# Kernel tuning notes

Hardware: AMD Instinct MI355X
Metric: run time of the kernel (lower is better)

The kernel has to match this reference:

```python
import jax, jax.numpy as jnp
import numpy as np

N = 50000      # nodes
E = 1600000    # edges (avg degree 32)
C_IN = 128
C_H = 128
C_OUT = 10
G = 512        # number of graphs in the batch


def setup_inputs() -> dict:
    key = jax.random.key(0)
    ks = jax.random.split(key, 16)
    x = jax.random.normal(ks[0], (N, C_IN), dtype=jnp.float32)
    edge_index = jax.random.randint(ks[1], (2, E), 0, N, dtype=jnp.int64)
    batch = jnp.sort(jax.random.randint(ks[2], (N,), 0, G, dtype=jnp.int64))

    def lin(k, fan_in, fan_out):
        lim = 1.0 / np.sqrt(fan_in)
        return jax.random.uniform(k, (fan_in, fan_out), jnp.float32, -lim, lim)

    return {
        "x": x, "edge_index": edge_index, "batch": batch,
        # conv1: c_in -> c_hidden
        "Wr1": lin(ks[3], C_IN, C_H), "br1": jnp.zeros((C_H,), jnp.float32),
        "Wo1": lin(ks[4], C_IN, C_H),
        # conv2: c_hidden -> 2*c_hidden
        "Wr2": lin(ks[5], C_H, 2 * C_H), "br2": jnp.zeros((2 * C_H,), jnp.float32),
        "Wo2": lin(ks[6], C_H, 2 * C_H),
        # conv3: 2*c_hidden -> c_hidden
        "Wr3": lin(ks[7], 2 * C_H, C_H), "br3": jnp.zeros((C_H,), jnp.float32),
        "Wo3": lin(ks[8], 2 * C_H, C_H),
        # head
        "W1": lin(ks[9], C_H, 4 * C_OUT), "b1": jnp.zeros((4 * C_OUT,), jnp.float32),
        "W2": lin(ks[10], 4 * C_OUT, C_OUT), "b2": jnp.zeros((C_OUT,), jnp.float32),
    }


def _graph_conv(x, src, dst, Wr, br, Wo):
    # PyG GraphConv: lin_rel(sum_{j in N(i)} x_j) + lin_root(x_i)
    agg = jax.ops.segment_sum(x[src], dst, num_segments=N)  # [N, F_in]
    return agg @ Wr + br + x @ Wo


def reference(x, edge_index, batch, Wr1, br1, Wo1, Wr2, br2, Wo2,
              Wr3, br3, Wo3, W1, b1, W2, b2):
    src, dst = edge_index[0], edge_index[1]
    h = jax.nn.relu(_graph_conv(x, src, dst, Wr1, br1, Wo1))
    h = jax.nn.relu(_graph_conv(h, src, dst, Wr2, br2, Wo2))
    h = _graph_conv(h, src, dst, Wr3, br3, Wo3)
    # global mean pool over graphs
    sums = jax.ops.segment_sum(h, batch, num_segments=G)            # [G, C_H]
    cnts = jax.ops.segment_sum(jnp.ones((N,), h.dtype), batch, num_segments=G)
    pooled = sums / jnp.maximum(cnts, 1.0)[:, None]
    # dropout is identity in eval mode
    out = pooled @ W1 + b1
    out = out @ W2 + b2
    return out
```

## Files before the change

kernel.cpp:

```cpp
#include <hip/hip_runtime.h>
#include <hip/hip_bf16.h>
#include <cstddef>

#define NN 50000
#define EE 1600000
#define GG 512
#define NB 196
#define BSTRIDE 16384
#define BCAP 10240
#define XBLKS 6250
#define SCBLKS 782
#define PSEG 8

typedef unsigned int u32;
typedef unsigned short u16;
typedef __attribute__((ext_vector_type(8))) short frag_ab;
typedef __attribute__((ext_vector_type(4))) float frag_cd;
typedef __attribute__((ext_vector_type(2))) float f32x2;

__device__ __forceinline__ void gl_lds16(const void* g, void* l) {
    __builtin_amdgcn_global_load_lds(
        (const __attribute__((address_space(1))) u32*)g,
        (__attribute__((address_space(3))) u32*)l, 16, 0, 0);
}
__device__ __forceinline__ float b2f_lo(u32 v) { return __uint_as_float(v << 16); }
__device__ __forceinline__ float b2f_hi(u32 v) { return __uint_as_float(v & 0xffff0000u); }
__device__ __forceinline__ float b2f(u32 v, int odd) { return odd ? b2f_hi(v) : b2f_lo(v); }
__device__ __forceinline__ u16 f2b(float x) {
    __hip_bfloat16 h = __float2bfloat16(x);
    return *(u16*)&h;
}
__device__ __forceinline__ u32 pack2(float lo, float hi) {
    return ((u32)f2b(hi) << 16) | f2b(lo);
}
__device__ __forceinline__ void accf8(float* a, u32 w) {
    f32x2 p0 = __builtin_amdgcn_cvt_pk_f32_fp8(w, false);
    f32x2 p1 = __builtin_amdgcn_cvt_pk_f32_fp8(w, true);
    a[0] += p0.x; a[1] += p0.y; a[2] += p1.x; a[3] += p1.y;
}
__device__ __forceinline__ u32 pk4_f8(float a, float b, float c, float d) {
    u32 w = __builtin_amdgcn_cvt_pk_fp8_f32(a, b, 0, false);
    return __builtin_amdgcn_cvt_pk_fp8_f32(c, d, w, true);
}

__device__ inline int lower_bound_i(const int* a, int n, int v) {
    int lo = 0, hi = n;
    while (lo < hi) {
        int m = (lo + hi) >> 1;
        if (a[m] < v) lo = m + 1; else hi = m;
    }
    return lo;
}



__global__ __launch_bounds__(256) void bscatter_prep_kernel(
    const int* __restrict__ ei, int* __restrict__ bcnt, u32* __restrict__ pairs,
    const float* __restrict__ x, u16* __restrict__ ax, u32* __restrict__ x8,
    const float* __restrict__ Wr1, const float* __restrict__ Wo1,
    const float* __restrict__ Wr2, const float* __restrict__ Wo2,
    const float* __restrict__ Wr3, const float* __restrict__ Wo3,
    const float* __restrict__ br3,
    u16* __restrict__ BT1, u16* __restrict__ BT2, u16* __restrict__ BT3,
    float* __restrict__ bias3, const int* __restrict__ batch,
    int* __restrict__ gn) {
    __shared__ int lcnt[NB];
    __shared__ int lbase[NB];
    __shared__ unsigned short lpos[2048];
    int bid = blockIdx.x, t = threadIdx.x;
    if (bid < SCBLKS) {
        int e0 = bid * 2048;
        u32 pk[8];
        int bk[8];
        for (int i = t; i < NB; i += 256) lcnt[i] = 0;
        __syncthreads();
#pragma unroll
        for (int i = 0; i < 8; ++i) {
            int e = e0 + i * 256 + t;
            if (e < EE) {
                int dst = ei[EE + e], src = ei[e];
                int b = dst >> 8;
                bk[i] = b;
                pk[i] = ((u32)src << 8) | (u32)(dst & 255);
                lpos[i * 256 + t] = (unsigned short)atomicAdd(&lcnt[b], 1);
            } else bk[i] = -1;
        }
        __syncthreads();
        for (int i = t; i < NB; i += 256) lbase[i] = atomicAdd(&bcnt[i], lcnt[i]);
        __syncthreads();
#pragma unroll
        for (int i = 0; i < 8; ++i) {
            if (bk[i] >= 0) {
                int pos = lbase[bk[i]] + (int)lpos[i * 256 + t];
                pairs[(size_t)bk[i] * BSTRIDE + pos] = pk[i];
            }
        }
    } else if (bid < SCBLKS + XBLKS) {
        int idx = (bid - SCBLKS) * 256 + t;
        int row = idx >> 5, q = idx & 31;
        float4 v = *(const float4*)(x + (size_t)row * 128 + q * 4);
        *(u32*)(ax + (size_t)row * 256 + 128 + q * 4) = pack2(v.x, v.y);
        *(u32*)(ax + (size_t)row * 256 + 128 + q * 4 + 2) = pack2(v.z, v.w);
        x8[(size_t)row * 32 + q] = pk4_f8(v.x, v.y, v.z, v.w);
    } else if (bid < SCBLKS + XBLKS + 256) {
        int m = bid - SCBLKS - XBLKS;
        int k = t;
        BT2[m * 256 + k] = f2b(k < 128 ? Wr2[k * 256 + m] : Wo2[(k - 128) * 256 + m]);
        BT3[m * 256 + k] = f2b(m < 128 ? Wr3[k * 128 + m] : Wo3[k * 128 + (m - 128)]);
        if (m < 128)
            BT1[m * 256 + k] = f2b(k < 128 ? Wr1[k * 128 + m] : Wo1[(k - 128) * 128 + m]);
        if (k == 0) bias3[m] = (m < 128) ? 0.f : br3[m - 128];
    } else {
        int g = (bid - SCBLKS - XBLKS - 256) * 256 + t;
        if (g <= GG) gn[g] = lower_bound_i(batch, NN, g);
    }
}


__global__ __launch_bounds__(1024) void bfill_kernel(const u32* __restrict__ pairs,
                                                     const int* __restrict__ bcnt,
                                                     int* __restrict__ ofs,
                                                     u16* __restrict__ srcl) {
    __shared__ int sc[256];
    __shared__ int cnts[256];
    __shared__ int lcnt[256];
    __shared__ int lcur[256];
    __shared__ int lbuf[BCAP];
    int b = blockIdx.x, t = threadIdx.x;
    if (t < 256) {
        int c = (t < NB) ? bcnt[t] : 0;
        cnts[t] = c;
        sc[t] = c;
        lcnt[t] = 0;
    }
    __syncthreads();
    for (int off = 1; off < 256; off <<= 1) {
        int v = (t >= off && t < 256) ? sc[t - off] : 0;
        __syncthreads();
        if (t < 256) sc[t] += v;
        __syncthreads();
    }
    int base = sc[b] - cnts[b];
    int span = cnts[b];
    const u32* pp = pairs + (size_t)b * BSTRIDE;
    for (int j = t; j < span; j += 1024) atomicAdd(&lcnt[pp[j] & 255u], 1);
    __syncthreads();
    int nc = 0;
    if (t < 256) {
        nc = lcnt[t];
        sc[t] = nc;
    }
    __syncthreads();
    for (int off = 1; off < 256; off <<= 1) {
        int v = (t >= off && t < 256) ? sc[t - off] : 0;
        __syncthreads();
        if (t < 256) sc[t] += v;
        __syncthreads();
    }
    if (t < 256) {
        int excl = sc[t] - nc;
        int node = b * 256 + t;
        if (node < NN) ofs[node] = base + excl;
        lcur[t] = excl;
    }
    if (b == 0 && t == 256) ofs[NN] = EE;
    __syncthreads();
    for (int j = t; j < span; j += 1024) {
        u32 p = pp[j];
        int pos = atomicAdd(&lcur[p & 255u], 1);
        int src = (int)(p >> 8);
        if (pos < BCAP) lbuf[pos] = src;
        else srcl[base + pos] = (u16)src;
    }
    __syncthreads();
    int lim = span < BCAP ? span : BCAP;
    for (int j = t; j < lim; j += 1024) srcl[base + j] = (u16)lbuf[j];
}


__global__ __launch_bounds__(256) void pull_f8_kernel(const u32* __restrict__ X8,
                                                      const int* __restrict__ ofs,
                                                      const u16* __restrict__ srcl,
                                                      u32* __restrict__ outu) {
    int node = (blockIdx.x * 256 + threadIdx.x) >> 6;
    int lane = threadIdx.x & 63;
    int q = lane >> 3, l = lane & 7;
    int lo = ofs[node], hi = ofs[node + 1];
    float acc[16];
#pragma unroll
    for (int i = 0; i < 16; ++i) acc[i] = 0.f;
    int j = lo;
    for (; j + 31 < hi; j += 32) {
        int s0 = srcl[j + q], s1 = srcl[j + 8 + q];
        int s2 = srcl[j + 16 + q], s3 = srcl[j + 24 + q];
        uint4 v0 = *(const uint4*)(X8 + (size_t)s0 * 32 + l * 4);
        uint4 v1 = *(const uint4*)(X8 + (size_t)s1 * 32 + l * 4);
        uint4 v2 = *(const uint4*)(X8 + (size_t)s2 * 32 + l * 4);
        uint4 v3 = *(const uint4*)(X8 + (size_t)s3 * 32 + l * 4);
        accf8(acc + 0, v0.x); accf8(acc + 4, v0.y); accf8(acc + 8, v0.z); accf8(acc + 12, v0.w);
        accf8(acc + 0, v1.x); accf8(acc + 4, v1.y); accf8(acc + 8, v1.z); accf8(acc + 12, v1.w);
        accf8(acc + 0, v2.x); accf8(acc + 4, v2.y); accf8(acc + 8, v2.z); accf8(acc + 12, v2.w);
        accf8(acc + 0, v3.x); accf8(acc + 4, v3.y); accf8(acc + 8, v3.z); accf8(acc + 12, v3.w);
    }
    if (j + 15 < hi) {
        int s0 = srcl[j + q], s1 = srcl[j + 8 + q];
        uint4 v0 = *(const uint4*)(X8 + (size_t)s0 * 32 + l * 4);
        uint4 v1 = *(const uint4*)(X8 + (size_t)s1 * 32 + l * 4);
        accf8(acc + 0, v0.x); accf8(acc + 4, v0.y); accf8(acc + 8, v0.z); accf8(acc + 12, v0.w);
        accf8(acc + 0, v1.x); accf8(acc + 4, v1.y); accf8(acc + 8, v1.z); accf8(acc + 12, v1.w);
        j += 16;
    }
    if (j + 7 < hi) {
        int s = srcl[j + q];
        uint4 v = *(const uint4*)(X8 + (size_t)s * 32 + l * 4);
        accf8(acc + 0, v.x); accf8(acc + 4, v.y); accf8(acc + 8, v.z); accf8(acc + 12, v.w);
        j += 8;
    }
    if (j + q < hi) {
        int s = srcl[j + q];
        uint4 v = *(const uint4*)(X8 + (size_t)s * 32 + l * 4);
        accf8(acc + 0, v.x); accf8(acc + 4, v.y); accf8(acc + 8, v.z); accf8(acc + 12, v.w);
    }
#pragma unroll
    for (int i = 0; i < 16; ++i) {
        acc[i] += __shfl_xor(acc[i], 8, 64);
        acc[i] += __shfl_xor(acc[i], 16, 64);
        acc[i] += __shfl_xor(acc[i], 32, 64);
    }
    if (q == 0) {
        uint4 r0, r1;
        r0.x = pack2(acc[0], acc[1]);  r0.y = pack2(acc[2], acc[3]);
        r0.z = pack2(acc[4], acc[5]);  r0.w = pack2(acc[6], acc[7]);
        r1.x = pack2(acc[8], acc[9]);  r1.y = pack2(acc[10], acc[11]);
        r1.z = pack2(acc[12], acc[13]); r1.w = pack2(acc[14], acc[15]);
        *(uint4*)(outu + (size_t)node * 128 + l * 8) = r0;
        *(uint4*)(outu + (size_t)node * 128 + l * 8 + 4) = r1;
    }
}


__global__ __launch_bounds__(256, 3) void gemm1_kernel(
    const u16* __restrict__ A, const u16* __restrict__ BT1,
    const float* __restrict__ br1, u16* __restrict__ C, u32* __restrict__ F8) {
    __shared__ alignas(16) u16 As[64 * 32];
    __shared__ alignas(16) u16 Bs[128 * 32];
    __shared__ alignas(16) u16 Hs[64 * 128];
    const int t = threadIdx.x;
    const int lane = t & 63, w = t >> 6;
    const int quad = lane >> 4, l16 = lane & 15;
    const int row0 = blockIdx.x * 64;

    const int ra = t >> 2, oa = (t & 3) * 8;
    const int garow = min(row0 + ra, NN - 1);
    const size_t gA = (size_t)garow * 256 + oa;
    size_t gB[2];
#pragma unroll
    for (int i = 0; i < 2; ++i) {
        int cbi = i * 256 + t;
        gB[i] = (size_t)(cbi >> 2) * 256 + (cbi & 3) * 8;
    }

    frag_cd acc[8];
#pragma unroll
    for (int i = 0; i < 8; ++i) acc[i] = (frag_cd)0.f;

    for (int kk = 0; kk < 256; kk += 32) {
        __syncthreads();
        gl_lds16(A + gA + kk, &As[t * 8]);
#pragma unroll
        for (int i = 0; i < 2; ++i)
            gl_lds16(BT1 + gB[i] + kk, &Bs[(i * 256 + t) * 8]);
        __syncthreads();
        frag_ab a = *(const frag_ab*)&As[(w * 16 + l16) * 32 + quad * 8];
#pragma unroll
        for (int nt = 0; nt < 8; ++nt) {
            frag_ab b = *(const frag_ab*)&Bs[(nt * 16 + l16) * 32 + quad * 8];
            acc[nt] = __builtin_amdgcn_mfma_f32_16x16x32_bf16(a, b, acc[nt], 0, 0, 0);
        }
    }
#pragma unroll
    for (int nt = 0; nt < 8; ++nt) {
        int col = nt * 16 + l16;
        float bv = br1[col];
#pragma unroll
        for (int r = 0; r < 4; ++r) {
            int lr = w * 16 + quad * 4 + r;
            float v = fmaxf(acc[nt][r] + bv, 0.f);
            Hs[(lr * 128 + col) ^ ((lr & 7) << 3)] = f2b(v);
        }
    }
    __syncthreads();
    const uint4* Hs128 = (const uint4*)Hs;
#pragma unroll
    for (int it = 0; it < 4; ++it) {
        int row = it * 16 + (t >> 4);
        int grp = t & 15;
        uint4 v = Hs128[row * 16 + (grp ^ (row & 7))];
        int grow = row0 + row;
        if (grow < NN) {
            *(uint4*)(C + (size_t)grow * 256 + 128 + grp * 8) = v;
            float f0 = b2f_lo(v.x), f1 = b2f_hi(v.x), f2 = b2f_lo(v.y), f3 = b2f_hi(v.y);
            float f4 = b2f_lo(v.z), f5 = b2f_hi(v.z), f6 = b2f_lo(v.w), f7 = b2f_hi(v.w);
            uint2 w8;
            w8.x = pk4_f8(f0, f1, f2, f3);
            w8.y = pk4_f8(f4, f5, f6, f7);
            *(uint2*)(F8 + (size_t)grow * 32 + grp * 2) = w8;
        }
    }
}


__global__ __launch_bounds__(256, 3) void gemm23_kernel(
    const u16* __restrict__ A, const u16* __restrict__ BT2,
    const float* __restrict__ br2, const u16* __restrict__ BT3,
    const float* __restrict__ bias3, u16* __restrict__ C, u32* __restrict__ T8) {
    __shared__ alignas(16) u16 As[64 * 32];
    __shared__ alignas(16) u16 Bs[256 * 32];
    __shared__ alignas(16) u16 Hs[64 * 256];
    const int t = threadIdx.x;
    const int lane = t & 63, w = t >> 6;
    const int quad = lane >> 4, l16 = lane & 15;
    const int row0 = blockIdx.x * 64;

    const int ra = t >> 2, oa = (t & 3) * 8;
    const int garow = min(row0 + ra, NN - 1);
    const size_t gA = (size_t)garow * 256 + oa;
    size_t gB[4];
#pragma unroll
    for (int i = 0; i < 4; ++i) {
        int cbi = i * 256 + t;
        gB[i] = (size_t)(cbi >> 2) * 256 + (cbi & 3) * 8;
    }

    frag_cd acc[16];
#pragma unroll
    for (int i = 0; i < 16; ++i) acc[i] = (frag_cd)0.f;

    for (int kk = 0; kk < 256; kk += 32) {
        __syncthreads();
        gl_lds16(A + gA + kk, &As[t * 8]);
#pragma unroll
        for (int i = 0; i < 4; ++i)
            gl_lds16(BT2 + gB[i] + kk, &Bs[(i * 256 + t) * 8]);
        __syncthreads();
        frag_ab a = *(const frag_ab*)&As[(w * 16 + l16) * 32 + quad * 8];
#pragma unroll
        for (int nt = 0; nt < 16; ++nt) {
            frag_ab b = *(const frag_ab*)&Bs[(nt * 16 + l16) * 32 + quad * 8];
            acc[nt] = __builtin_amdgcn_mfma_f32_16x16x32_bf16(a, b, acc[nt], 0, 0, 0);
        }
    }
#pragma unroll
    for (int nt = 0; nt < 16; ++nt) {
        int col = nt * 16 + l16;
        float bv = br2[col];
#pragma unroll
        for (int r = 0; r < 4; ++r) {
            int lr = w * 16 + quad * 4 + r;
            float v = fmaxf(acc[nt][r] + bv, 0.f);
            Hs[(lr * 256 + col) ^ ((lr & 7) << 3)] = f2b(v);
        }
    }

#pragma unroll
    for (int i = 0; i < 16; ++i) acc[i] = (frag_cd)0.f;
    const int hrow = w * 16 + l16;
    for (int kk = 0; kk < 256; kk += 32) {
        __syncthreads();
#pragma unroll
        for (int i = 0; i < 4; ++i)
            gl_lds16(BT3 + gB[i] + kk, &Bs[(i * 256 + t) * 8]);
        __syncthreads();
        frag_ab a = *(const frag_ab*)&Hs[(hrow * 256 + kk + quad * 8) ^
                                         ((hrow & 7) << 3)];
#pragma unroll
        for (int nt = 0; nt < 16; ++nt) {
            frag_ab b = *(const frag_ab*)&Bs[(nt * 16 + l16) * 32 + quad * 8];
            acc[nt] = __builtin_amdgcn_mfma_f32_16x16x32_bf16(a, b, acc[nt], 0, 0, 0);
        }
    }

#pragma unroll
    for (int nt = 0; nt < 16; ++nt) {
        int col = nt * 16 + l16;
        float bv = bias3[col];
#pragma unroll
        for (int r = 0; r < 4; ++r) {
            int lr = w * 16 + quad * 4 + r;
            Hs[(lr * 256 + col) ^ ((lr & 7) << 3)] = f2b(acc[nt][r] + bv);
        }
    }
    __syncthreads();
    const uint4* Hs128 = (const uint4*)Hs;
#pragma unroll
    for (int it = 0; it < 8; ++it) {
        int row = it * 8 + (t >> 5);
        int grp = t & 31;
        uint4 v = Hs128[row * 32 + (grp ^ (row & 7))];
        int grow = row0 + row;
        if (grow < NN)
            *(uint4*)(C + (size_t)grow * 256 + grp * 8) = v;
    }
#pragma unroll
    for (int it = 0; it < 4; ++it) {
        int row = it * 16 + (t >> 4);
        int grp = t & 15;
        uint4 v = Hs128[row * 32 + (grp ^ (row & 7))];
        int grow = row0 + row;
        if (grow < NN) {
            float f0 = b2f_lo(v.x), f1 = b2f_hi(v.x), f2 = b2f_lo(v.y), f3 = b2f_hi(v.y);
            float f4 = b2f_lo(v.z), f5 = b2f_hi(v.z), f6 = b2f_lo(v.w), f7 = b2f_hi(v.w);
            uint2 w8;
            w8.x = pk4_f8(f0, f1, f2, f3);
            w8.y = pk4_f8(f4, f5, f6, f7);
            *(uint2*)(T8 + (size_t)grow * 32 + grp * 2) = w8;
        }
    }
}


__global__ __launch_bounds__(256) void pool3_f8_kernel(
    const u32* __restrict__ T8, const u32* __restrict__ Tu,
    const int* __restrict__ ofs, const u16* __restrict__ srcl,
    const int* __restrict__ gn, float* __restrict__ psum) {
    __shared__ float red[4][128];
    __shared__ float po[2][128];
    int gb = blockIdx.x;
    int g = gb >> 3, s = gb & 7;
    int t = threadIdx.x;
    int w = t >> 6, lane = t & 63;
    int q = lane >> 3, l = lane & 7;
    int n_lo = gn[g], n_hi = gn[g + 1];
    int glo = ofs[n_lo], ghi = ofs[n_hi];
    int len = ghi - glo;
    int s_lo = glo + (int)(((long long)len * s) >> 3);
    int s_hi = glo + (int)(((long long)len * (s + 1)) >> 3);
    int slen = s_hi - s_lo;
    int wlo = s_lo + ((slen * w) >> 2);
    int whi = s_lo + ((slen * (w + 1)) >> 2);

    float acc[16];
#pragma unroll
    for (int i = 0; i < 16; ++i) acc[i] = 0.f;
    int j = wlo;
    for (; j + 31 < whi; j += 32) {
        int s0 = srcl[j + q], s1 = srcl[j + 8 + q];
        int s2 = srcl[j + 16 + q], s3 = srcl[j + 24 + q];
        uint4 v0 = *(const uint4*)(T8 + (size_t)s0 * 32 + l * 4);
        uint4 v1 = *(const uint4*)(T8 + (size_t)s1 * 32 + l * 4);
        uint4 v2 = *(const uint4*)(T8 + (size_t)s2 * 32 + l * 4);
        uint4 v3 = *(const uint4*)(T8 + (size_t)s3 * 32 + l * 4);
        accf8(acc + 0, v0.x); accf8(acc + 4, v0.y); accf8(acc + 8, v0.z); accf8(acc + 12, v0.w);
        accf8(acc + 0, v1.x); accf8(acc + 4, v1.y); accf8(acc + 8, v1.z); accf8(acc + 12, v1.w);
        accf8(acc + 0, v2.x); accf8(acc + 4, v2.y); accf8(acc + 8, v2.z); accf8(acc + 12, v2.w);
        accf8(acc + 0, v3.x); accf8(acc + 4, v3.y); accf8(acc + 8, v3.z); accf8(acc + 12, v3.w);
    }
    if (j + 15 < whi) {
        int s0 = srcl[j + q], s1 = srcl[j + 8 + q];
        uint4 v0 = *(const uint4*)(T8 + (size_t)s0 * 32 + l * 4);
        uint4 v1 = *(const uint4*)(T8 + (size_t)s1 * 32 + l * 4);
        accf8(acc + 0, v0.x); accf8(acc + 4, v0.y); accf8(acc + 8, v0.z); accf8(acc + 12, v0.w);
        accf8(acc + 0, v1.x); accf8(acc + 4, v1.y); accf8(acc + 8, v1.z); accf8(acc + 12, v1.w);
        j += 16;
    }
    if (j + 7 < whi) {
        int sv = srcl[j + q];
        uint4 v = *(const uint4*)(T8 + (size_t)sv * 32 + l * 4);
        accf8(acc + 0, v.x); accf8(acc + 4, v.y); accf8(acc + 8, v.z); accf8(acc + 12, v.w);
        j += 8;
    }
    if (j + q < whi) {
        int sv = srcl[j + q];
        uint4 v = *(const uint4*)(T8 + (size_t)sv * 32 + l * 4);
        accf8(acc + 0, v.x); accf8(acc + 4, v.y); accf8(acc + 8, v.z); accf8(acc + 12, v.w);
    }
#pragma unroll
    for (int i = 0; i < 16; ++i) {
        acc[i] += __shfl_xor(acc[i], 8, 64);
        acc[i] += __shfl_xor(acc[i], 16, 64);
        acc[i] += __shfl_xor(acc[i], 32, 64);
    }
    if (q == 0) {
#pragma unroll
        for (int i = 0; i < 16; ++i) red[w][l * 16 + i] = acc[i];
    }
    float so = 0.f;
    int ch = t & 127, rg = t >> 7;
    for (int r = n_lo + s * 2 + rg; r < n_hi; r += 16)
        so += b2f(Tu[(size_t)r * 128 + 64 + (ch >> 1)], ch & 1);
    po[rg][ch] = so;
    __syncthreads();
    if (t < 128) {
        float v = red[0][t] + red[1][t] + red[2][t] + red[3][t] + po[0][t] + po[1][t];
        psum[((size_t)g * PSEG + s) * 128 + t] = v;
    }
}


__global__ __launch_bounds__(128) void head_kernel(
    const float* __restrict__ psum, const int* __restrict__ gn,
    const float* __restrict__ W1, const float* __restrict__ b1,
    const float* __restrict__ W2, const float* __restrict__ b2,
    float* __restrict__ out) {
    __shared__ float p[128];
    __shared__ float hid[40];
    int g = blockIdx.x, t = threadIdx.x;
    int cnt = gn[g + 1] - gn[g];
    float sv = 0.f;
#pragma unroll
    for (int k = 0; k < PSEG; ++k) sv += psum[((size_t)g * PSEG + k) * 128 + t];
    p[t] = sv / fmaxf((float)cnt, 1.f);
    __syncthreads();
    if (t < 40) {
        float v = b1[t];
        for (int k = 0; k < 128; ++k) v += p[k] * W1[k * 40 + t];
        hid[t] = v;
    }
    __syncthreads();
    if (t < 10) {
        float v = b2[t];
        for (int j = 0; j < 40; ++j) v += hid[j] * W2[j * 10 + t];
        out[g * 10 + t] = v;
    }
}


extern "C" void kernel_launch(void* const* d_in, const int* in_sizes, int n_in,
                              void* d_out, int out_size, void* d_ws, size_t ws_size,
                              hipStream_t stream) {
    const float* x   = (const float*)d_in[0];
    const int* ei    = (const int*)d_in[1];
    const int* batch = (const int*)d_in[2];
    const float* Wr1 = (const float*)d_in[3];
    const float* br1 = (const float*)d_in[4];
    const float* Wo1 = (const float*)d_in[5];
    const float* Wr2 = (const float*)d_in[6];
    const float* br2 = (const float*)d_in[7];
    const float* Wo2 = (const float*)d_in[8];
    const float* Wr3 = (const float*)d_in[9];
    const float* br3 = (const float*)d_in[10];
    const float* Wo3 = (const float*)d_in[11];
    const float* W1  = (const float*)d_in[12];
    const float* b1  = (const float*)d_in[13];
    const float* W2  = (const float*)d_in[14];
    const float* b2  = (const float*)d_in[15];
    float* out = (float*)d_out;

    char* ws = (char*)d_ws;
    size_t off = 0;
    auto alloc = [&](size_t bytes) {
        void* p = ws + off;
        off += (bytes + 255) & ~(size_t)255;
        return p;
    };
    int* ofs      = (int*)alloc((NN + 1) * sizeof(int));
    int* bcnt     = (int*)alloc(256 * sizeof(int));
    int* gn       = (int*)alloc((GG + 1) * sizeof(int));
    u16* srcl     = (u16*)alloc((size_t)EE * 2);
    u16* ax       = (u16*)alloc((size_t)NN * 256 * 2);
    u16* ah1      = (u16*)alloc((size_t)NN * 256 * 2);
    u16* t3o3     = (u16*)alloc((size_t)NN * 256 * 2);
    u32* x8       = (u32*)alloc((size_t)NN * 128);
    u32* h1f8     = (u32*)alloc((size_t)NN * 128);
    u32* t3f8     = (u32*)alloc((size_t)NN * 128);
    float* psum   = (float*)alloc((size_t)GG * PSEG * 128 * sizeof(float));
    u16* BT1      = (u16*)alloc(128 * 256 * 2);
    u16* BT2      = (u16*)alloc(256 * 256 * 2);
    u16* BT3      = (u16*)alloc(256 * 256 * 2);
    float* bias3  = (float*)alloc(256 * sizeof(float));
    u32* pairs = (u32*)t3o3;

    hipMemsetAsync(bcnt, 0, 256 * sizeof(int), stream);

    bscatter_prep_kernel<<<SCBLKS + XBLKS + 256 + 3, 256, 0, stream>>>(
        ei, bcnt, pairs, x, ax, x8, Wr1, Wo1, Wr2, Wo2, Wr3, Wo3, br3,
        BT1, BT2, BT3, bias3, batch, gn);
    bfill_kernel<<<NB, 1024, 0, stream>>>(pairs, bcnt, ofs, srcl);

    pull_f8_kernel<<<NN * 64 / 256, 256, 0, stream>>>(x8, ofs, srcl, (u32*)ax);
    gemm1_kernel<<<782, 256, 0, stream>>>(ax, BT1, br1, ah1, h1f8);
    pull_f8_kernel<<<NN * 64 / 256, 256, 0, stream>>>(h1f8, ofs, srcl, (u32*)ah1);
    gemm23_kernel<<<782, 256, 0, stream>>>(ah1, BT2, br2, BT3, bias3, t3o3, t3f8);

    pool3_f8_kernel<<<GG * PSEG, 256, 0, stream>>>(t3f8, (const u32*)t3o3,
                                                   ofs, srcl, gn, psum);
    head_kernel<<<GG, 128, 0, stream>>>(psum, gn, W1, b1, W2, b2, out);
}
```

Before: 301.3 us.

## Double-buffer LDS tiles in GEMM kernels to overlap loads with MFMA

Both GEMM kernels now keep two LDS buffers for the A/B tiles. The next k-slice is prefetched while MFMAs run on the current one, cutting one barrier per iteration, and the layer-3 weight prefetch is chained onto the end of the layer-2 loop. Occupancy hints change (gemm1 up to 4 blocks per CU, gemm23 down to 2) because LDS use grows. The fp8 epilogue is merged into the bf16 store loop so Hs is read once. The larger LDS footprint may lower occupancy for gemm23, and these GEMMs are probably a small part of a runtime dominated by the gather/scatter kernels.

After: 296.6 us. No clear change (-1.6%).

```diff
diff --git a/kernel.cpp b/kernel.cpp
--- a/kernel.cpp
+++ b/kernel.cpp
@@ -239,11 +239,11 @@
 }
 
 
-__global__ __launch_bounds__(256, 3) void gemm1_kernel(
+__global__ __launch_bounds__(256, 4) void gemm1_kernel(
     const u16* __restrict__ A, const u16* __restrict__ BT1,
     const float* __restrict__ br1, u16* __restrict__ C, u32* __restrict__ F8) {
-    __shared__ alignas(16) u16 As[64 * 32];
-    __shared__ alignas(16) u16 Bs[128 * 32];
+    __shared__ alignas(16) u16 As[2][64 * 32];
+    __shared__ alignas(16) u16 Bs[2][128 * 32];
     __shared__ alignas(16) u16 Hs[64 * 128];
     const int t = threadIdx.x;
     const int lane = t & 63, w = t >> 6;
@@ -264,19 +264,28 @@
 #pragma unroll
     for (int i = 0; i < 8; ++i) acc[i] = (frag_cd)0.f;
 
+    gl_lds16(A + gA, &As[0][t * 8]);
+#pragma unroll
+    for (int i = 0; i < 2; ++i)
+        gl_lds16(BT1 + gB[i], &Bs[0][(i * 256 + t) * 8]);
+    __syncthreads();
+
+    int buf = 0;
     for (int kk = 0; kk < 256; kk += 32) {
-        __syncthreads();
-        gl_lds16(A + gA + kk, &As[t * 8]);
-#pragma unroll
-        for (int i = 0; i < 2; ++i)
-            gl_lds16(BT1 + gB[i] + kk, &Bs[(i * 256 + t) * 8]);
-        __syncthreads();
-        frag_ab a = *(const frag_ab*)&As[(w * 16 + l16) * 32 + quad * 8];
+        if (kk < 224) {
+            gl_lds16(A + gA + kk + 32, &As[buf ^ 1][t * 8]);
+#pragma unroll
+            for (int i = 0; i < 2; ++i)
+                gl_lds16(BT1 + gB[i] + kk + 32, &Bs[buf ^ 1][(i * 256 + t) * 8]);
+        }
+        frag_ab a = *(const frag_ab*)&As[buf][(w * 16 + l16) * 32 + quad * 8];
 #pragma unroll
         for (int nt = 0; nt < 8; ++nt) {
-            frag_ab b = *(const frag_ab*)&Bs[(nt * 16 + l16) * 32 + quad * 8];
+            frag_ab b = *(const frag_ab*)&Bs[buf][(nt * 16 + l16) * 32 + quad * 8];
             acc[nt] = __builtin_amdgcn_mfma_f32_16x16x32_bf16(a, b, acc[nt], 0, 0, 0);
         }
+        __syncthreads();
+        buf ^= 1;
     }
 #pragma unroll
     for (int nt = 0; nt < 8; ++nt) {
@@ -310,12 +319,12 @@
 }
 
 
-__global__ __launch_bounds__(256, 3) void gemm23_kernel(
+__global__ __launch_bounds__(256, 2) void gemm23_kernel(
     const u16* __restrict__ A, const u16* __restrict__ BT2,
     const float* __restrict__ br2, const u16* __restrict__ BT3,
     const float* __restrict__ bias3, u16* __restrict__ C, u32* __restrict__ T8) {
-    __shared__ alignas(16) u16 As[64 * 32];
-    __shared__ alignas(16) u16 Bs[256 * 32];
+    __shared__ alignas(16) u16 As[2][64 * 32];
+    __shared__ alignas(16) u16 Bs[2][256 * 32];
     __shared__ alignas(16) u16 Hs[64 * 256];
     const int t = threadIdx.x;
     const int lane = t & 63, w = t >> 6;
@@ -336,19 +345,32 @@
 #pragma unroll
     for (int i = 0; i < 16; ++i) acc[i] = (frag_cd)0.f;
 
+    gl_lds16(A + gA, &As[0][t * 8]);
+#pragma unroll
+    for (int i = 0; i < 4; ++i)
+        gl_lds16(BT2 + gB[i], &Bs[0][(i * 256 + t) * 8]);
+    __syncthreads();
+
+    int buf = 0;
     for (int kk = 0; kk < 256; kk += 32) {
-        __syncthreads();
-        gl_lds16(A + gA + kk, &As[t * 8]);
-#pragma unroll
-        for (int i = 0; i < 4; ++i)
-            gl_lds16(BT2 + gB[i] + kk, &Bs[(i * 256 + t) * 8]);
-        __syncthreads();
-        frag_ab a = *(const frag_ab*)&As[(w * 16 + l16) * 32 + quad * 8];
+        if (kk < 224) {
+            gl_lds16(A + gA + kk + 32, &As[buf ^ 1][t * 8]);
+#pragma unroll
+            for (int i = 0; i < 4; ++i)
+                gl_lds16(BT2 + gB[i] + kk + 32, &Bs[buf ^ 1][(i * 256 + t) * 8]);
+        } else {
+#pragma unroll
+            for (int i = 0; i < 4; ++i)
+                gl_lds16(BT3 + gB[i], &Bs[buf ^ 1][(i * 256 + t) * 8]);
+        }
+        frag_ab a = *(const frag_ab*)&As[buf][(w * 16 + l16) * 32 + quad * 8];
 #pragma unroll
         for (int nt = 0; nt < 16; ++nt) {
-            frag_ab b = *(const frag_ab*)&Bs[(nt * 16 + l16) * 32 + quad * 8];
+            frag_ab b = *(const frag_ab*)&Bs[buf][(nt * 16 + l16) * 32 + quad * 8];
             acc[nt] = __builtin_amdgcn_mfma_f32_16x16x32_bf16(a, b, acc[nt], 0, 0, 0);
         }
+        __syncthreads();
+        buf ^= 1;
     }
 #pragma unroll
     for (int nt = 0; nt < 16; ++nt) {
@@ -366,18 +388,20 @@
     for (int i = 0; i < 16; ++i) acc[i] = (frag_cd)0.f;
     const int hrow = w * 16 + l16;
     for (int kk = 0; kk < 256; kk += 32) {
-        __syncthreads();
-#pragma unroll
-        for (int i = 0; i < 4; ++i)
-            gl_lds16(BT3 + gB[i] + kk, &Bs[(i * 256 + t) * 8]);
-        __syncthreads();
+        if (kk < 224) {
+#pragma unroll
+            for (int i = 0; i < 4; ++i)
+                gl_lds16(BT3 + gB[i] + kk + 32, &Bs[buf ^ 1][(i * 256 + t) * 8]);
+        }
         frag_ab a = *(const frag_ab*)&Hs[(hrow * 256 + kk + quad * 8) ^
                                          ((hrow & 7) << 3)];
 #pragma unroll
         for (int nt = 0; nt < 16; ++nt) {
-            frag_ab b = *(const frag_ab*)&Bs[(nt * 16 + l16) * 32 + quad * 8];
+            frag_ab b = *(const frag_ab*)&Bs[buf][(nt * 16 + l16) * 32 + quad * 8];
             acc[nt] = __builtin_amdgcn_mfma_f32_16x16x32_bf16(a, b, acc[nt], 0, 0, 0);
         }
+        __syncthreads();
+        buf ^= 1;
     }
 
 #pragma unroll
@@ -398,22 +422,16 @@
         int grp = t & 31;
         uint4 v = Hs128[row * 32 + (grp ^ (row & 7))];
         int grow = row0 + row;
-        if (grow < NN)
+        if (grow < NN) {
             *(uint4*)(C + (size_t)grow * 256 + grp * 8) = v;
-    }
-#pragma unroll
-    for (int it = 0; it < 4; ++it) {
-        int row = it * 16 + (t >> 4);
-        int grp = t & 15;
-        uint4 v = Hs128[row * 32 + (grp ^ (row & 7))];
-        int grow = row0 + row;
-        if (grow < NN) {
-            float f0 = b2f_lo(v.x), f1 = b2f_hi(v.x), f2 = b2f_lo(v.y), f3 = b2f_hi(v.y);
-            float f4 = b2f_lo(v.z), f5 = b2f_hi(v.z), f6 = b2f_lo(v.w), f7 = b2f_hi(v.w);
-            uint2 w8;
-            w8.x = pk4_f8(f0, f1, f2, f3);
-            w8.y = pk4_f8(f4, f5, f6, f7);
-            *(uint2*)(T8 + (size_t)grow * 32 + grp * 2) = w8;
+            if (grp < 16) {
+                float f0 = b2f_lo(v.x), f1 = b2f_hi(v.x), f2 = b2f_lo(v.y), f3 = b2f_hi(v.y);
+                float f4 = b2f_lo(v.z), f5 = b2f_hi(v.z), f6 = b2f_lo(v.w), f7 = b2f_hi(v.w);
+                uint2 w8;
+                w8.x = pk4_f8(f0, f1, f2, f3);
+                w8.y = pk4_f8(f4, f5, f6, f7);
+                *(uint2*)(T8 + (size_t)grow * 32 + grp * 2) = w8;
+            }
         }
     }
 }
```
